# Kernel tuning notes

Hardware: AMD Instinct MI355X
Metric: run time of the kernel (lower is better)

The kernel has to match this reference:

```python
import jax, jax.numpy as jnp
import numpy as np

B, S, D = 2, 2048, 2048
H, KVH, HD = 8, 1, 256          # query heads, kv heads, head_dim (GQA: n_rep = H // KVH)
ROPE_THETA = 10000.0
NEG_INF = -1e9


def setup_inputs() -> dict:
    key = jax.random.key(0)
    k1, k2, k3, k4, k5 = jax.random.split(key, 5)
    hidden_states = jax.random.normal(k1, (B, S, D), dtype=jnp.float32)
    # additive causal mask: 0 where allowed, -inf where masked, shape (B,1,S,S)
    causal = jnp.tril(jnp.ones((S, S), dtype=bool))
    attention_mask = jnp.where(causal, 0.0, NEG_INF).astype(jnp.float32)
    attention_mask = jnp.broadcast_to(attention_mask[None, None], (B, 1, S, S))
    position_ids = jnp.broadcast_to(jnp.arange(S, dtype=jnp.int32)[None, :], (B, S))
    sc = 0.02
    Wq = jax.random.normal(k2, (H * HD, D), dtype=jnp.float32) * sc   # torch Linear weight layout [out,in]
    Wk = jax.random.normal(k3, (KVH * HD, D), dtype=jnp.float32) * sc
    Wv = jax.random.normal(k4, (KVH * HD, D), dtype=jnp.float32) * sc
    Wo = jax.random.normal(k5, (D, H * HD), dtype=jnp.float32) * sc
    return {"hidden_states": hidden_states, "attention_mask": attention_mask,
            "position_ids": position_ids, "Wq": Wq, "Wk": Wk, "Wv": Wv, "Wo": Wo}


def _rotate_half(x):
    x1, x2 = jnp.split(x, 2, axis=-1)
    return jnp.concatenate((-x2, x1), axis=-1)


def _rope_cos_sin(position_ids):
    inv_freq = 1.0 / (ROPE_THETA ** (jnp.arange(0, HD, 2, dtype=jnp.float32) / HD))  # [HD/2]
    freqs = position_ids.astype(jnp.float32)[:, :, None] * inv_freq[None, None, :]   # [B,S,HD/2]
    emb = jnp.concatenate((freqs, freqs), axis=-1)                                   # [B,S,HD]
    return jnp.cos(emb)[:, None], jnp.sin(emb)[:, None]                              # [B,1,S,HD]


def reference(hidden_states, attention_mask, position_ids, Wq, Wk, Wv, Wo):
    q = (hidden_states @ Wq.T).reshape(B, S, H, HD).transpose(0, 2, 1, 3)     # [B,H,S,HD]
    k = (hidden_states @ Wk.T).reshape(B, S, KVH, HD).transpose(0, 2, 1, 3)   # [B,KVH,S,HD]
    v = (hidden_states @ Wv.T).reshape(B, S, KVH, HD).transpose(0, 2, 1, 3)
    cos, sin = _rope_cos_sin(position_ids)
    q = q * cos + _rotate_half(q) * sin
    k = k * cos + _rotate_half(k) * sin
    n_rep = H // KVH
    k = jnp.repeat(k, n_rep, axis=1)                                          # repeat_kv -> [B,H,S,HD]
    v = jnp.repeat(v, n_rep, axis=1)
    scores = jnp.einsum('bhqd,bhkd->bhqk', q, k) / jnp.sqrt(jnp.float32(HD))
    scores = scores + attention_mask
    attn = jax.nn.softmax(scores, axis=-1)                                    # dropout p=0 (eval)
    ctx = jnp.einsum('bhqk,bhkd->bhqd', attn, v)
    ctx = ctx.transpose(0, 2, 1, 3).reshape(B, S, H * HD)
    out = ctx @ Wo.T
    return out, attn
```

## Files before the change

### kernel.cpp

```cpp
#include <hip/hip_runtime.h>
#include <hip/hip_bf16.h>
#include <math.h>

typedef __bf16 bf16_t;
typedef __bf16 bf16x8 __attribute__((ext_vector_type(8)));
typedef float  f32x4  __attribute__((ext_vector_type(4)));

#define DEV __device__ __forceinline__

constexpr int B_   = 2;
constexpr int S_   = 2048;
constexpr int D_   = 2048;
constexpr int H_   = 8;
constexpr int HD_  = 256;
constexpr int NQKV_ = H_ * HD_ + 2 * HD_;
constexpr int TOK_ = B_ * S_;
constexpr int CHK_ = 64 * HD_;

#if defined(__has_builtin)
#if __has_builtin(__builtin_amdgcn_global_load_lds)
#define HAS_GLLDS 1
#endif
#endif

DEV void stage16(const bf16_t* g, bf16_t* l) {
#ifdef HAS_GLLDS
  __builtin_amdgcn_global_load_lds((const __attribute__((address_space(1))) void*)g,
                                   (__attribute__((address_space(3))) void*)l, 16, 0, 0);
#else
  *(bf16x8*)l = *(const bf16x8*)g;
#endif
}

__global__ void cast_inputs(const float* __restrict__ hs, const float* __restrict__ wq,
                            const float* __restrict__ wk, const float* __restrict__ wv,
                            const float* __restrict__ wo,
                            bf16_t* __restrict__ Xb, bf16_t* __restrict__ Wqkvb,
                            bf16_t* __restrict__ Wob) {
  const size_t i = (size_t)blockIdx.x * blockDim.x + threadIdx.x;
  const size_t NHS = (size_t)TOK_ * D_;
  const size_t NWQ = (size_t)H_ * HD_ * D_;
  const size_t NWK = (size_t)HD_ * D_;
  if (i < NHS) Xb[i] = (bf16_t)hs[i];
  if (i < NWQ) { Wqkvb[i] = (bf16_t)wq[i]; Wob[i] = (bf16_t)wo[i]; }
  if (i < NWK) { Wqkvb[NWQ + i] = (bf16_t)wk[i]; Wqkvb[NWQ + NWK + i] = (bf16_t)wv[i]; }
}

DEV void tile_k64(const bf16_t* __restrict__ Ab, const bf16_t* __restrict__ Bg,
                  int K, int lda, int ldb, int m0, int n0,
                  bf16_t* Asm, bf16_t* Bsm, f32x4 acc[4][4],
                  int tid, int lrow, int quad, int wm, int wn)
{
  const int sw = (lrow & 1) << 2;
  for (int k0 = 0; k0 < K; k0 += 64) {
    __syncthreads();
    #pragma unroll
    for (int c = 0; c < 4; ++c) {
      int chunk = c * 256 + tid;
      int row = chunk >> 3, pg = chunk & 7;
      int g = pg ^ ((row & 1) << 2);
      stage16(Ab + (size_t)(m0 + row) * lda + (k0 + g * 8), &Asm[chunk * 8]);
      stage16(Bg + (size_t)(n0 + row) * ldb + (k0 + g * 8), &Bsm[chunk * 8]);
    }
    __syncthreads();
    #pragma unroll
    for (int kk = 0; kk < 2; ++kk) {
      bf16x8 af[4], bfr[4];
      #pragma unroll
      for (int i = 0; i < 4; ++i)
        af[i] = *(const bf16x8*)&Asm[(wm + i * 16 + lrow) * 64 + ((quad + kk * 4) ^ sw) * 8];
      #pragma unroll
      for (int j = 0; j < 4; ++j)
        bfr[j] = *(const bf16x8*)&Bsm[(wn + j * 16 + lrow) * 64 + ((quad + kk * 4) ^ sw) * 8];
      #pragma unroll
      for (int i = 0; i < 4; ++i)
        #pragma unroll
        for (int j = 0; j < 4; ++j)
          acc[i][j] = __builtin_amdgcn_mfma_f32_16x16x32_bf16(af[i], bfr[j], acc[i][j], 0, 0, 0);
    }
  }
}

template <bool CBF16>
__global__ __launch_bounds__(256, 2)
void gemm_bt(const bf16_t* __restrict__ Ab, const bf16_t* __restrict__ Bg,
             void* __restrict__ Cv, int K, int lda, int ldb, int ldc)
{
  const int nwg = gridDim.x * gridDim.y;
  const int w0  = blockIdx.y * gridDim.x + blockIdx.x;
  const int q   = nwg >> 3;
  const int logical = (w0 & 7) * q + (w0 >> 3);
  const int bm = logical / gridDim.x, bn = logical % gridDim.x;
  const int m0 = bm * 128, n0 = bn * 128;

  __shared__ __align__(16) bf16_t Asm[128 * 64];
  __shared__ __align__(16) bf16_t Bsm[128 * 64];

  const int tid  = threadIdx.x;
  const int l    = tid & 63;
  const int w    = tid >> 6;
  const int wm   = (w >> 1) * 64;
  const int wn   = (w & 1) * 64;
  const int lrow = l & 15;
  const int quad = l >> 4;

  f32x4 acc[4][4] = {};
  tile_k64(Ab, Bg, K, lda, ldb, m0, n0, Asm, Bsm, acc, tid, lrow, quad, wm, wn);

  #pragma unroll
  for (int i = 0; i < 4; ++i) {
    int row = wm + i * 16 + quad * 4;
    #pragma unroll
    for (int j = 0; j < 4; ++j) {
      int col = n0 + wn + j * 16 + lrow;
      #pragma unroll
      for (int r = 0; r < 4; ++r) {
        if (CBF16) ((bf16_t*)Cv)[(size_t)(m0 + row + r) * ldc + col] = (bf16_t)acc[i][j][r];
        else       ((float*) Cv)[(size_t)(m0 + row + r) * ldc + col] = acc[i][j][r];
      }
    }
  }
}

__global__ void rope_kernel(const bf16_t* __restrict__ qkv, const int* __restrict__ pos_ids,
                            bf16_t* __restrict__ Qh, bf16_t* __restrict__ Kb,
                            bf16_t* __restrict__ K2)
{
  const int t = blockIdx.x;
  const int b = t >> 11, s = t & (S_ - 1);
  const int tid = threadIdx.x;
  const int h = tid >> 5, c = tid & 31;
  const float pos = (float)pos_ids[t];
  const int pdbase = (c & 15) * 8;
  float cs[8], sn[8];
  #pragma unroll
  for (int j = 0; j < 8; ++j) {
    float invf = exp2f((float)(pdbase + j) * -0.103810253f);
    float ang = pos * invf;
    cs[j] = cosf(ang); sn[j] = sinf(ang);
  }
  const float sgn = (c < 16) ? -1.0f : 1.0f;
  const bf16_t* base = qkv + (size_t)t * NQKV_;

  {
    bf16x8 x  = *(const bf16x8*)(base + h * HD_ + c * 8);
    bf16x8 xo = *(const bf16x8*)(base + h * HD_ + (c ^ 16) * 8);
    bf16x8 o;
    #pragma unroll
    for (int j = 0; j < 8; ++j)
      o[j] = (bf16_t)((float)x[j] * cs[j] + sgn * (float)xo[j] * sn[j]);
    *(bf16x8*)(Qh + ((size_t)(b * H_ + h) * S_ + s) * HD_ + c * 8) = o;
  }
  if (h == 0) {
    bf16x8 x  = *(const bf16x8*)(base + D_ + c * 8);
    bf16x8 xo = *(const bf16x8*)(base + D_ + (c ^ 16) * 8);
    bf16x8 o;
    #pragma unroll
    for (int j = 0; j < 8; ++j)
      o[j] = (bf16_t)((float)x[j] * cs[j] + sgn * (float)xo[j] * sn[j]);
    *(bf16x8*)(Kb + (size_t)t * HD_ + c * 8) = o;
    const int chunk = s >> 6, key = s & 63;
    *(bf16x8*)(K2 + (size_t)(b * 32 + chunk) * CHK_ + c * 512 + key * 8) = o;
  }
}

__global__ void v_trans(const bf16_t* __restrict__ qkv, bf16_t* __restrict__ V2)
{
  const int blk = blockIdx.x;
  const int s0 = (blk & 31) * 64;
  const int b = blk >> 5;
  const int tid = threadIdx.x;
  __shared__ bf16_t L[64][264];
  #pragma unroll
  for (int it = 0; it < 8; ++it) {
    int gi = it * 256 + tid;
    int r = gi >> 5, cc = gi & 31;
    *(bf16x8*)&L[r][cc * 8] =
        *(const bf16x8*)(qkv + ((size_t)b * S_ + s0 + r) * NQKV_ + (D_ + HD_) + cc * 8);
  }
  __syncthreads();
  bf16_t* out = V2 + (size_t)blk * CHK_;
  #pragma unroll
  for (int it = 0; it < 8; ++it) {
    int G = it * 256 + tid;
    bf16x8 o;
    #pragma unroll
    for (int j = 0; j < 8; ++j) o[j] = L[it * 8 + j][tid];
    *(bf16x8*)(out + (size_t)G * 8) = o;
  }
}

constexpr int PSTR = 136;

DEV void compute_S(const bf16_t* __restrict__ K2g, bf16_t* __restrict__ KV,
                   const bf16x8 aq[8], f32x4 accS[8],
                   int kb, int tid, int lrow, int quad)
{
  #pragma unroll
  for (int half = 0; half < 2; ++half) {
    __syncthreads();
    const bf16_t* src = K2g + (size_t)(kb * 2 + half) * CHK_;
    #pragma unroll
    for (int it = 0; it < 8; ++it) {
      int s = it * 256 + tid;
      stage16(src + (size_t)s * 8, KV + s * 8);
    }
    __syncthreads();
    __builtin_amdgcn_s_setprio(1);
    #pragma unroll
    for (int kk = 0; kk < 8; ++kk) {
      bf16x8 bk[4];
      #pragma unroll
      for (int j = 0; j < 4; ++j)
        bk[j] = *(const bf16x8*)&KV[((kk * 4 + quad) * 64 + j * 16 + lrow) * 8];
      #pragma unroll
      for (int j = 0; j < 4; ++j)
        accS[half * 4 + j] =
            __builtin_amdgcn_mfma_f32_16x16x32_bf16(aq[kk], bk[j], accS[half * 4 + j], 0, 0, 0);
    }
    __builtin_amdgcn_s_setprio(0);
  }
}

__global__ __launch_bounds__(256, 2)
void flash_attn(const bf16_t* __restrict__ Qh, const bf16_t* __restrict__ K2,
                const bf16_t* __restrict__ V2, bf16_t* __restrict__ Ctx,
                float* __restrict__ lsum)
{
  const int idx = blockIdx.x;
  int z, qb;
  if (idx < 256) { z = idx & 15; qb = idx >> 4; }
  else           { int j = idx - 256; z = j & 15; qb = 31 - (j >> 4); }
  const int b = z >> 3, h = z & 7;
  const int q0 = qb * 64;
  const bf16_t* Qg  = Qh + ((size_t)z * S_ + q0) * HD_;
  const bf16_t* K2g = K2 + (size_t)b * 32 * CHK_;
  const bf16_t* V2g = V2 + (size_t)b * 32 * CHK_;

  __shared__ __align__(16) bf16_t KV[64 * 256];
  __shared__ __align__(16) bf16_t Pst[4 * 16 * PSTR];

  const int tid = threadIdx.x;
  const int w = tid >> 6, l = tid & 63;
  const int lrow = l & 15, quad = l >> 4;
  const int nkb = (qb >> 1) + 1;
  const float scale = 0.0625f;

  bf16x8 aq[8];
  const bf16_t* qrow = Qg + (size_t)(w * 16 + lrow) * HD_ + quad * 8;
  #pragma unroll
  for (int kk = 0; kk < 8; ++kk) aq[kk] = *(const bf16x8*)(qrow + kk * 32);

  const int rowg0 = q0 + w * 16 + quad * 4;
  float lp[4] = {0.f, 0.f, 0.f, 0.f};
  f32x4 accO[16] = {};
  bf16_t* pw = &Pst[w * 16 * PSTR];

  for (int kb = 0; kb < nkb; ++kb) {
    f32x4 accS[8] = {};
    compute_S(K2g, KV, aq, accS, kb, tid, lrow, quad);
    __syncthreads();

    {
      const bf16_t* src = V2g + (size_t)(kb * 2 + 0) * CHK_;
      #pragma unroll
      for (int it = 0; it < 8; ++it) {
        int s = it * 256 + tid;
        stage16(src + (size_t)s * 8, KV + s * 8);
      }
    }

    #pragma unroll
    for (int r = 0; r < 4; ++r) {
      #pragma unroll
      for (int j = 0; j < 8; ++j) {
        int col = kb * 128 + j * 16 + lrow;
        float p = (col <= rowg0 + r) ? __expf(accS[j][r] * scale) : 0.f;
        lp[r] += p;
        pw[(quad * 4 + r) * PSTR + j * 16 + lrow] = (bf16_t)p;
      }
    }
    bf16x8 ap[4];
    #pragma unroll
    for (int kk2 = 0; kk2 < 4; ++kk2)
      ap[kk2] = *(const bf16x8*)&pw[lrow * PSTR + kk2 * 32 + quad * 8];

    __syncthreads();
    __builtin_amdgcn_s_setprio(1);
    #pragma unroll
    for (int kkl = 0; kkl < 2; ++kkl) {
      #pragma unroll
      for (int j2 = 0; j2 < 16; ++j2) {
        bf16x8 bv = *(const bf16x8*)&KV[((kkl * 4 + quad) * 256 + j2 * 16 + lrow) * 8];
        accO[j2] = __builtin_amdgcn_mfma_f32_16x16x32_bf16(ap[kkl], bv, accO[j2], 0, 0, 0);
      }
    }
    __builtin_amdgcn_s_setprio(0);

    __syncthreads();
    {
      const bf16_t* src = V2g + (size_t)(kb * 2 + 1) * CHK_;
      #pragma unroll
      for (int it = 0; it < 8; ++it) {
        int s = it * 256 + tid;
        stage16(src + (size_t)s * 8, KV + s * 8);
      }
    }
    __syncthreads();
    __builtin_amdgcn_s_setprio(1);
    #pragma unroll
    for (int kkl = 0; kkl < 2; ++kkl) {
      #pragma unroll
      for (int j2 = 0; j2 < 16; ++j2) {
        bf16x8 bv = *(const bf16x8*)&KV[((kkl * 4 + quad) * 256 + j2 * 16 + lrow) * 8];
        accO[j2] = __builtin_amdgcn_mfma_f32_16x16x32_bf16(ap[2 + kkl], bv, accO[j2], 0, 0, 0);
      }
    }
    __builtin_amdgcn_s_setprio(0);
  }

  #pragma unroll
  for (int r = 0; r < 4; ++r) {
    #pragma unroll
    for (int o = 1; o < 16; o <<= 1) lp[r] += __shfl_xor(lp[r], o, 64);
  }
  float inv[4];
  #pragma unroll
  for (int r = 0; r < 4; ++r) inv[r] = 1.0f / lp[r];

  #pragma unroll
  for (int j2 = 0; j2 < 16; ++j2) {
    #pragma unroll
    for (int r = 0; r < 4; ++r) {
      int rowq = q0 + w * 16 + quad * 4 + r;
      Ctx[((size_t)b * S_ + rowq) * D_ + h * HD_ + j2 * 16 + lrow] = (bf16_t)(accO[j2][r] * inv[r]);
    }
  }
  if (lrow == 0) {
    #pragma unroll
    for (int r = 0; r < 4; ++r) lsum[(size_t)z * S_ + rowg0 + r] = lp[r];
  }
}

__global__ __launch_bounds__(256, 2)
void p_writer(const bf16_t* __restrict__ Qh, const bf16_t* __restrict__ Kbp,
              const float* __restrict__ lsum, float* __restrict__ attn)
{
  const int w0 = (blockIdx.z * gridDim.y + blockIdx.y) * gridDim.x + blockIdx.x;
  const int logical = (w0 & 7) * 512 + (w0 >> 3);
  const int z = logical >> 8, bm = (logical >> 4) & 15, bn = logical & 15;
  const int m0 = bm * 128, n0 = bn * 128;
  float* Pg = attn + (size_t)z * S_ * S_;
  const int tid = threadIdx.x;

  if (bn > bm) {
    #pragma unroll
    for (int it = 0; it < 16; ++it) {
      int idx = it * 256 + tid;
      int row = idx >> 5, c4 = idx & 31;
      *(f32x4*)&Pg[(size_t)(m0 + row) * S_ + n0 + c4 * 4] = f32x4{0.f, 0.f, 0.f, 0.f};
    }
    return;
  }

  const bf16_t* Ab = Qh + (size_t)z * S_ * HD_;
  const bf16_t* Bg = Kbp + (size_t)(z >> 3) * S_ * HD_;

  __shared__ __align__(16) bf16_t Asm[128 * 64];
  __shared__ __align__(16) bf16_t Bsm[128 * 64];

  const int l    = tid & 63;
  const int w    = tid >> 6;
  const int wm   = (w >> 1) * 64;
  const int wn   = (w & 1) * 64;
  const int lrow = l & 15;
  const int quad = l >> 4;

  f32x4 acc[4][4] = {};
  tile_k64(Ab, Bg, HD_, HD_, HD_, m0, n0, Asm, Bsm, acc, tid, lrow, quad, wm, wn);

  const float scale = 0.0625f;
  #pragma unroll
  for (int i = 0; i < 4; ++i) {
    int row = m0 + wm + i * 16 + quad * 4;
    #pragma unroll
    for (int r = 0; r < 4; ++r) {
      const float il = 1.0f / lsum[(size_t)z * S_ + row + r];
      float* prow = &Pg[(size_t)(row + r) * S_];
      #pragma unroll
      for (int j = 0; j < 4; ++j) {
        int col = n0 + wn + j * 16 + lrow;
        prow[col] = (col <= row + r) ? __expf(acc[i][j][r] * scale) * il : 0.f;
      }
    }
  }
}

extern "C" void kernel_launch(void* const* d_in, const int* in_sizes, int n_in,
                              void* d_out, int out_size, void* d_ws, size_t ws_size,
                              hipStream_t stream)
{
  const float* hs  = (const float*)d_in[0];
  const int*   pos = (const int*)d_in[2];
  const float* wq  = (const float*)d_in[3];
  const float* wk  = (const float*)d_in[4];
  const float* wv  = (const float*)d_in[5];
  const float* wo  = (const float*)d_in[6];

  float* out  = (float*)d_out;
  float* attn = out + (size_t)TOK_ * D_;

  char* ws = (char*)d_ws;
  bf16_t* Xb    = (bf16_t*)(ws);
  bf16_t* Wqkvb = (bf16_t*)(ws + 16777216);
  bf16_t* Wob   = (bf16_t*)(ws + 27262976);
  bf16_t* QKVb  = (bf16_t*)(ws + 35651584);
  bf16_t* Qh    = (bf16_t*)(ws + 56623104);
  bf16_t* Kb    = (bf16_t*)(ws + 73400320);
  bf16_t* V2    = (bf16_t*)(ws + 75497472);
  bf16_t* Ctx   = (bf16_t*)(ws + 77594624);
  float*  lsum  = (float* )(ws + 94371840);
  bf16_t* K2    = (bf16_t*)(ws + 94502912);

  cast_inputs<<<(TOK_ * D_) / 256, 256, 0, stream>>>(hs, wq, wk, wv, wo, Xb, Wqkvb, Wob);
  gemm_bt<true><<<dim3(NQKV_ / 128, TOK_ / 128), 256, 0, stream>>>(
      Xb, Wqkvb, QKVb, D_, D_, D_, NQKV_);
  rope_kernel<<<TOK_, 256, 0, stream>>>(QKVb, pos, Qh, Kb, K2);
  v_trans<<<B_ * 32, 256, 0, stream>>>(QKVb, V2);
  flash_attn<<<512, 256, 0, stream>>>(Qh, K2, V2, Ctx, lsum);
  p_writer<<<dim3(S_ / 128, S_ / 128, B_ * H_), 256, 0, stream>>>(Qh, Kb, lsum, attn);
  gemm_bt<false><<<dim3(D_ / 128, TOK_ / 128), 256, 0, stream>>>(
      Ctx, Wob, out, D_, D_, D_, D_);
}
```

Measured before the change: 591.0 us.

## Store unnormalized P from flash attention and normalize in a streaming pass

Flash attention now writes its bf16 exponentiated scores to a workspace buffer. A new row-wise kernel scales them by the inverse row sum and writes the fp32 attention matrix with zeros above the diagonal. This replaces the separate p_writer kernel, which recomputed QK^T with MFMA, and removes the extra K buffer. The cost is a bf16 intermediate write and read of the full causal score matrix, plus extra global stores inside the attention loop.

```diff
diff --git a/kernel.cpp b/kernel.cpp
--- a/kernel.cpp
+++ b/kernel.cpp
@@ -123,8 +123,7 @@
 }
 
 __global__ void rope_kernel(const bf16_t* __restrict__ qkv, const int* __restrict__ pos_ids,
-                            bf16_t* __restrict__ Qh, bf16_t* __restrict__ Kb,
-                            bf16_t* __restrict__ K2)
+                            bf16_t* __restrict__ Qh, bf16_t* __restrict__ K2)
 {
   const int t = blockIdx.x;
   const int b = t >> 11, s = t & (S_ - 1);
@@ -158,7 +157,6 @@
     #pragma unroll
     for (int j = 0; j < 8; ++j)
       o[j] = (bf16_t)((float)x[j] * cs[j] + sgn * (float)xo[j] * sn[j]);
-    *(bf16x8*)(Kb + (size_t)t * HD_ + c * 8) = o;
     const int chunk = s >> 6, key = s & 63;
     *(bf16x8*)(K2 + (size_t)(b * 32 + chunk) * CHK_ + c * 512 + key * 8) = o;
   }
@@ -225,7 +223,7 @@
 __global__ __launch_bounds__(256, 2)
 void flash_attn(const bf16_t* __restrict__ Qh, const bf16_t* __restrict__ K2,
                 const bf16_t* __restrict__ V2, bf16_t* __restrict__ Ctx,
-                float* __restrict__ lsum)
+                bf16_t* __restrict__ P2, float* __restrict__ lsum)
 {
   const int idx = blockIdx.x;
   int z, qb;
@@ -236,6 +234,7 @@
   const bf16_t* Qg  = Qh + ((size_t)z * S_ + q0) * HD_;
   const bf16_t* K2g = K2 + (size_t)b * 32 * CHK_;
   const bf16_t* V2g = V2 + (size_t)b * 32 * CHK_;
+  bf16_t* P2g = P2 + (size_t)z * S_ * S_;
 
   __shared__ __align__(16) bf16_t KV[64 * 256];
   __shared__ __align__(16) bf16_t Pst[4 * 16 * PSTR];
@@ -297,6 +296,14 @@
     }
     __builtin_amdgcn_s_setprio(0);
 
+    #pragma unroll
+    for (int it = 0; it < 4; ++it) {
+      int chunk = it * 256 + tid;
+      int prow = chunk >> 4, g = chunk & 15;
+      bf16x8 pv = *(const bf16x8*)&Pst[prow * PSTR + g * 8];
+      *(bf16x8*)(P2g + (size_t)(q0 + prow) * S_ + kb * 128 + g * 8) = pv;
+    }
+
     __syncthreads();
     {
       const bf16_t* src = V2g + (size_t)(kb * 2 + 1) * CHK_;
@@ -342,58 +349,27 @@
   }
 }
 
-__global__ __launch_bounds__(256, 2)
-void p_writer(const bf16_t* __restrict__ Qh, const bf16_t* __restrict__ Kbp,
-              const float* __restrict__ lsum, float* __restrict__ attn)
-{
-  const int w0 = (blockIdx.z * gridDim.y + blockIdx.y) * gridDim.x + blockIdx.x;
-  const int logical = (w0 & 7) * 512 + (w0 >> 3);
-  const int z = logical >> 8, bm = (logical >> 4) & 15, bn = logical & 15;
-  const int m0 = bm * 128, n0 = bn * 128;
-  float* Pg = attn + (size_t)z * S_ * S_;
+__global__ __launch_bounds__(256)
+void normalize_attn(const bf16_t* __restrict__ P2, const float* __restrict__ lsum,
+                    float* __restrict__ attn)
+{
+  const int row = blockIdx.x & (S_ - 1);
+  const int z   = blockIdx.x >> 11;
   const int tid = threadIdx.x;
-
-  if (bn > bm) {
-    #pragma unroll
-    for (int it = 0; it < 16; ++it) {
-      int idx = it * 256 + tid;
-      int row = idx >> 5, c4 = idx & 31;
-      *(f32x4*)&Pg[(size_t)(m0 + row) * S_ + n0 + c4 * 4] = f32x4{0.f, 0.f, 0.f, 0.f};
-    }
-    return;
-  }
-
-  const bf16_t* Ab = Qh + (size_t)z * S_ * HD_;
-  const bf16_t* Bg = Kbp + (size_t)(z >> 3) * S_ * HD_;
-
-  __shared__ __align__(16) bf16_t Asm[128 * 64];
-  __shared__ __align__(16) bf16_t Bsm[128 * 64];
-
-  const int l    = tid & 63;
-  const int w    = tid >> 6;
-  const int wm   = (w >> 1) * 64;
-  const int wn   = (w & 1) * 64;
-  const int lrow = l & 15;
-  const int quad = l >> 4;
-
-  f32x4 acc[4][4] = {};
-  tile_k64(Ab, Bg, HD_, HD_, HD_, m0, n0, Asm, Bsm, acc, tid, lrow, quad, wm, wn);
-
-  const float scale = 0.0625f;
-  #pragma unroll
-  for (int i = 0; i < 4; ++i) {
-    int row = m0 + wm + i * 16 + quad * 4;
-    #pragma unroll
-    for (int r = 0; r < 4; ++r) {
-      const float il = 1.0f / lsum[(size_t)z * S_ + row + r];
-      float* prow = &Pg[(size_t)(row + r) * S_];
-      #pragma unroll
-      for (int j = 0; j < 4; ++j) {
-        int col = n0 + wn + j * 16 + lrow;
-        prow[col] = (col <= row + r) ? __expf(acc[i][j][r] * scale) * il : 0.f;
-      }
-    }
-  }
+  const float il = 1.0f / lsum[(size_t)z * S_ + row];
+  const bf16_t* src = P2 + ((size_t)z * S_ + row) * S_;
+  float* dst = attn + ((size_t)z * S_ + row) * S_;
+  const int c0 = tid * 8;
+  f32x4 o0 = {0.f, 0.f, 0.f, 0.f}, o1 = {0.f, 0.f, 0.f, 0.f};
+  if (c0 <= row) {
+    bf16x8 p = *(const bf16x8*)(src + c0);
+    #pragma unroll
+    for (int j = 0; j < 4; ++j) o0[j] = (c0 + j <= row) ? (float)p[j] * il : 0.f;
+    #pragma unroll
+    for (int j = 0; j < 4; ++j) o1[j] = (c0 + 4 + j <= row) ? (float)p[4 + j] * il : 0.f;
+  }
+  *(f32x4*)(dst + c0) = o0;
+  *(f32x4*)(dst + c0 + 4) = o1;
 }
 
 extern "C" void kernel_launch(void* const* d_in, const int* in_sizes, int n_in,
@@ -416,19 +392,19 @@
   bf16_t* Wob   = (bf16_t*)(ws + 27262976);
   bf16_t* QKVb  = (bf16_t*)(ws + 35651584);
   bf16_t* Qh    = (bf16_t*)(ws + 56623104);
-  bf16_t* Kb    = (bf16_t*)(ws + 73400320);
   bf16_t* V2    = (bf16_t*)(ws + 75497472);
   bf16_t* Ctx   = (bf16_t*)(ws + 77594624);
   float*  lsum  = (float* )(ws + 94371840);
   bf16_t* K2    = (bf16_t*)(ws + 94502912);
+  bf16_t* P2    = (bf16_t*)(ws + 100663296);
 
   cast_inputs<<<(TOK_ * D_) / 256, 256, 0, stream>>>(hs, wq, wk, wv, wo, Xb, Wqkvb, Wob);
   gemm_bt<true><<<dim3(NQKV_ / 128, TOK_ / 128), 256, 0, stream>>>(
       Xb, Wqkvb, QKVb, D_, D_, D_, NQKV_);
-  rope_kernel<<<TOK_, 256, 0, stream>>>(QKVb, pos, Qh, Kb, K2);
+  rope_kernel<<<TOK_, 256, 0, stream>>>(QKVb, pos, Qh, K2);
   v_trans<<<B_ * 32, 256, 0, stream>>>(QKVb, V2);
-  flash_attn<<<512, 256, 0, stream>>>(Qh, K2, V2, Ctx, lsum);
-  p_writer<<<dim3(S_ / 128, S_ / 128, B_ * H_), 256, 0, stream>>>(Qh, Kb, lsum, attn);
+  flash_attn<<<512, 256, 0, stream>>>(Qh, K2, V2, Ctx, P2, lsum);
+  normalize_attn<<<16 * S_, 256, 0, stream>>>(P2, lsum, attn);
   gemm_bt<false><<<dim3(D_ / 128, TOK_ / 128), 256, 0, stream>>>(
       Ctx, Wob, out, D_, D_, D_, D_);
 }
```

Result: slower. 614.3 us (+3.9%).

## Double-buffer LDS tiles in bf16 GEMM mainloop to overlap loads with MFMA

Applied to the files above, without the earlier changes.

Replaces the single-buffered K-loop with a double-buffered version that issues global-to-LDS loads for the next K tile before computing on the current one. This drops one barrier per iteration and lets memory traffic overlap with matrix-core work in both the projection GEMMs and the attention-probability kernel. It doubles LDS use per block (64KB), which may limit occupancy against the launch bound of 2 blocks per CU.

```diff
diff --git a/kernel.cpp b/kernel.cpp
--- a/kernel.cpp
+++ b/kernel.cpp
@@ -46,32 +46,49 @@
   if (i < NWK) { Wqkvb[NWQ + i] = (bf16_t)wk[i]; Wqkvb[NWQ + NWK + i] = (bf16_t)wv[i]; }
 }
 
-DEV void tile_k64(const bf16_t* __restrict__ Ab, const bf16_t* __restrict__ Bg,
-                  int K, int lda, int ldb, int m0, int n0,
-                  bf16_t* Asm, bf16_t* Bsm, f32x4 acc[4][4],
-                  int tid, int lrow, int quad, int wm, int wn)
+DEV void tile_k64_db(const bf16_t* __restrict__ Ab, const bf16_t* __restrict__ Bg,
+                     int K, int lda, int ldb, int m0, int n0,
+                     bf16_t* Asm, bf16_t* Bsm,
+                     f32x4 acc[4][4],
+                     int tid, int lrow, int quad, int wm, int wn)
 {
   const int sw = (lrow & 1) << 2;
-  for (int k0 = 0; k0 < K; k0 += 64) {
-    __syncthreads();
-    #pragma unroll
-    for (int c = 0; c < 4; ++c) {
-      int chunk = c * 256 + tid;
-      int row = chunk >> 3, pg = chunk & 7;
-      int g = pg ^ ((row & 1) << 2);
-      stage16(Ab + (size_t)(m0 + row) * lda + (k0 + g * 8), &Asm[chunk * 8]);
-      stage16(Bg + (size_t)(n0 + row) * ldb + (k0 + g * 8), &Bsm[chunk * 8]);
-    }
-    __syncthreads();
+  int srow[4], sg[4];
+  #pragma unroll
+  for (int c = 0; c < 4; ++c) {
+    int chunk = c * 256 + tid;
+    srow[c] = chunk >> 3;
+    sg[c]   = (chunk & 7) ^ ((srow[c] & 1) << 2);
+  }
+  #pragma unroll
+  for (int c = 0; c < 4; ++c) {
+    int chunk = c * 256 + tid;
+    stage16(Ab + (size_t)(m0 + srow[c]) * lda + sg[c] * 8, &Asm[chunk * 8]);
+    stage16(Bg + (size_t)(n0 + srow[c]) * ldb + sg[c] * 8, &Bsm[chunk * 8]);
+  }
+  const int nT = K >> 6;
+  for (int t = 0; t < nT; ++t) {
+    const int cur = (t & 1) * (128 * 64);
+    const int nxt = ((t + 1) & 1) * (128 * 64);
+    __syncthreads();
+    if (t + 1 < nT) {
+      const int k0 = (t + 1) << 6;
+      #pragma unroll
+      for (int c = 0; c < 4; ++c) {
+        int chunk = c * 256 + tid;
+        stage16(Ab + (size_t)(m0 + srow[c]) * lda + (k0 + sg[c] * 8), &Asm[nxt + chunk * 8]);
+        stage16(Bg + (size_t)(n0 + srow[c]) * ldb + (k0 + sg[c] * 8), &Bsm[nxt + chunk * 8]);
+      }
+    }
     #pragma unroll
     for (int kk = 0; kk < 2; ++kk) {
       bf16x8 af[4], bfr[4];
       #pragma unroll
       for (int i = 0; i < 4; ++i)
-        af[i] = *(const bf16x8*)&Asm[(wm + i * 16 + lrow) * 64 + ((quad + kk * 4) ^ sw) * 8];
+        af[i] = *(const bf16x8*)&Asm[cur + (wm + i * 16 + lrow) * 64 + ((quad + kk * 4) ^ sw) * 8];
       #pragma unroll
       for (int j = 0; j < 4; ++j)
-        bfr[j] = *(const bf16x8*)&Bsm[(wn + j * 16 + lrow) * 64 + ((quad + kk * 4) ^ sw) * 8];
+        bfr[j] = *(const bf16x8*)&Bsm[cur + (wn + j * 16 + lrow) * 64 + ((quad + kk * 4) ^ sw) * 8];
       #pragma unroll
       for (int i = 0; i < 4; ++i)
         #pragma unroll
@@ -93,8 +110,8 @@
   const int bm = logical / gridDim.x, bn = logical % gridDim.x;
   const int m0 = bm * 128, n0 = bn * 128;
 
-  __shared__ __align__(16) bf16_t Asm[128 * 64];
-  __shared__ __align__(16) bf16_t Bsm[128 * 64];
+  __shared__ __align__(16) bf16_t Asm[2 * 128 * 64];
+  __shared__ __align__(16) bf16_t Bsm[2 * 128 * 64];
 
   const int tid  = threadIdx.x;
   const int l    = tid & 63;
@@ -105,7 +122,7 @@
   const int quad = l >> 4;
 
   f32x4 acc[4][4] = {};
-  tile_k64(Ab, Bg, K, lda, ldb, m0, n0, Asm, Bsm, acc, tid, lrow, quad, wm, wn);
+  tile_k64_db(Ab, Bg, K, lda, ldb, m0, n0, Asm, Bsm, acc, tid, lrow, quad, wm, wn);
 
   #pragma unroll
   for (int i = 0; i < 4; ++i) {
@@ -366,8 +383,8 @@
   const bf16_t* Ab = Qh + (size_t)z * S_ * HD_;
   const bf16_t* Bg = Kbp + (size_t)(z >> 3) * S_ * HD_;
 
-  __shared__ __align__(16) bf16_t Asm[128 * 64];
-  __shared__ __align__(16) bf16_t Bsm[128 * 64];
+  __shared__ __align__(16) bf16_t Asm[2 * 128 * 64];
+  __shared__ __align__(16) bf16_t Bsm[2 * 128 * 64];
 
   const int l    = tid & 63;
   const int w    = tid >> 6;
@@ -377,7 +394,7 @@
   const int quad = l >> 4;
 
   f32x4 acc[4][4] = {};
-  tile_k64(Ab, Bg, HD_, HD_, HD_, m0, n0, Asm, Bsm, acc, tid, lrow, quad, wm, wn);
+  tile_k64_db(Ab, Bg, HD_, HD_, HD_, m0, n0, Asm, Bsm, acc, tid, lrow, quad, wm, wn);
 
   const float scale = 0.0625f;
   #pragma unroll
```

Measured after the change: 616.1 us. 1.04x slower.
